# Optimization experiments

Measured on AMD Instinct MI355X. Metric: run time of the kernel, lower is better.

## Reference

```python
import jax, jax.numpy as jnp
import numpy as np

B, S, E = 2, 2048, 1024
H, HKV = 16, 4
D = E // H          # head_dim = 64
REP = H // HKV      # kv repeat factor = 4


def setup_inputs() -> dict:
    key = jax.random.key(0)
    ks = jax.random.split(key, 9)
    std = 0.02
    x = jax.random.normal(ks[0], (B, S, E), dtype=jnp.float32)
    # causal mask: True means masked (upper triangle, strictly above diagonal)
    mask = jnp.triu(jnp.ones((S, S), dtype=bool), k=1)
    wq_w = jax.random.normal(ks[1], (E, E), dtype=jnp.float32) * std
    wq_b = jax.random.normal(ks[2], (E,), dtype=jnp.float32) * std
    wk_w = jax.random.normal(ks[3], (HKV * D, E), dtype=jnp.float32) * std
    wk_b = jax.random.normal(ks[4], (HKV * D,), dtype=jnp.float32) * std
    wv_w = jax.random.normal(ks[5], (HKV * D, E), dtype=jnp.float32) * std
    wv_b = jax.random.normal(ks[6], (HKV * D,), dtype=jnp.float32) * std
    wo_w = jax.random.normal(ks[7], (E, E), dtype=jnp.float32) * std
    wo_b = jax.random.normal(ks[8], (E,), dtype=jnp.float32) * std
    return {"x": x, "mask": mask, "wq_w": wq_w, "wq_b": wq_b,
            "wk_w": wk_w, "wk_b": wk_b, "wv_w": wv_w, "wv_b": wv_b,
            "wo_w": wo_w, "wo_b": wo_b}


def reference(x, mask, wq_w, wq_b, wk_w, wk_b, wv_w, wv_b, wo_w, wo_b):
    b, s, e = x.shape
    # projections (torch Linear: x @ W.T + b)
    q = x @ wq_w.T + wq_b                       # [B,S,E]
    k = x @ wk_w.T + wk_b                       # [B,S,HKV*D]
    v = x @ wv_w.T + wv_b
    # q grouped by kv head: [B, HKV, REP, S, D]; k/v: [B, HKV, S, D]
    q = q.reshape(b, s, HKV, REP, D).transpose(0, 2, 3, 1, 4)
    k = k.reshape(b, s, HKV, D).transpose(0, 2, 1, 3)
    v = v.reshape(b, s, HKV, D).transpose(0, 2, 1, 3)
    scale = D ** (-0.5)
    # scores [B, HKV, REP, Sq, Skv] -- same math as physical repeat_kv
    scores = jnp.einsum('bgrsd,bgtd->bgrst', q, k) * scale
    scores = jnp.where(mask, -jnp.inf, scores)
    w = jax.nn.softmax(scores, axis=-1)
    ctx = jnp.einsum('bgrst,bgtd->bgrsd', w, v)  # [B,HKV,REP,S,D]
    ctx = ctx.transpose(0, 3, 1, 2, 4).reshape(b, s, e)
    return ctx @ wo_w.T + wo_b
```

## Files before the change

kernel.cpp:

```cpp
#include <hip/hip_runtime.h>


typedef __attribute__((ext_vector_type(8))) short bh8;
typedef __attribute__((ext_vector_type(4))) short sh4;
typedef __attribute__((ext_vector_type(4))) float fv4;
typedef __attribute__((ext_vector_type(2))) unsigned int uv2;

#define MFMA16 __builtin_amdgcn_mfma_f32_16x16x32_bf16

static __device__ __forceinline__ float fast_exp2(float x) {
  return __builtin_amdgcn_exp2f(x);
}
static __device__ __forceinline__ unsigned short f2bf(float f) {
  unsigned int u; __builtin_memcpy(&u, &f, 4);
  u += 0x7fffu + ((u >> 16) & 1u);
  return (unsigned short)(u >> 16);
}
static __device__ __forceinline__ unsigned int pack2(float a, float b) {
  unsigned int r;
  asm("v_cvt_pk_bf16_f32 %0, %1, %2" : "=v"(r) : "v"(a), "v"(b));
  return r;
}
static __device__ __forceinline__ void gload16(const short* g, short* l) {
  __builtin_amdgcn_global_load_lds(
      (const __attribute__((address_space(1))) void*)g,
      (__attribute__((address_space(3))) void*)l, 16, 0, 0);
}

static __device__ __forceinline__ bh8 pshuf(const float* p, int quad, int l16) {
  unsigned int u01 = pack2(p[0], p[1]);
  unsigned int u23 = pack2(p[2], p[3]);
  unsigned int u45 = pack2(p[4], p[5]);
  unsigned int u67 = pack2(p[6], p[7]);
  const int g0 = (((quad << 1)    ) & 3) * 16 + l16;
  const int g1 = (((quad << 1) + 1) & 3) * 16 + l16;
  unsigned int w0l = __shfl((int)u01, g0), w0h = __shfl((int)u45, g0);
  unsigned int w1l = __shfl((int)u23, g0), w1h = __shfl((int)u67, g0);
  unsigned int w2l = __shfl((int)u01, g1), w2h = __shfl((int)u45, g1);
  unsigned int w3l = __shfl((int)u23, g1), w3h = __shfl((int)u67, g1);
  const bool up = (quad & 2) != 0;
  union { unsigned int w[4]; bh8 v; } pu;
  pu.w[0] = up ? w0h : w0l;
  pu.w[1] = up ? w1h : w1l;
  pu.w[2] = up ? w2h : w2l;
  pu.w[3] = up ? w3h : w3l;
  return pu.v;
}

__global__ __launch_bounds__(256) void cvt_all(
    const float* __restrict__ x,  const float* __restrict__ wq,
    const float* __restrict__ wk, const float* __restrict__ wv,
    const float* __restrict__ wo,
    short* __restrict__ xb, short* __restrict__ wqkvb, short* __restrict__ wob)
{
  const int i = blockIdx.x * 256 + threadIdx.x;
  const float* src; short* dst; int j;
  if (i < 1048576)      { j = i;           src = x;  dst = xb; }
  else if (i < 1310720) { j = i - 1048576; src = wq; dst = wqkvb; }
  else if (i < 1376256) { j = i - 1310720; src = wk; dst = wqkvb + (size_t)1024 * 1024; }
  else if (i < 1441792) { j = i - 1376256; src = wv; dst = wqkvb + (size_t)1280 * 1024; }
  else                  { j = i - 1441792; src = wo; dst = wob; }
  const float4 v = ((const float4*)src)[j];
  sh4 o = { (short)f2bf(v.x), (short)f2bf(v.y),
            (short)f2bf(v.z), (short)f2bf(v.w) };
  ((sh4*)dst)[j] = o;
}

__global__ __launch_bounds__(256) void gemm_dbuf(
    const short* __restrict__ A, const short* __restrict__ W,
    const float* __restrict__ biasQ, const float* __restrict__ biasK,
    const float* __restrict__ biasV,
    short* __restrict__ Cq, short* __restrict__ Ck, short* __restrict__ Cvt,
    float* __restrict__ Cf,
    int M, int K, int S, int mode, float scaleQ)
{
  __shared__ short As[2][128 * 64];
  __shared__ short Bs[2][64 * 64];
  const int tid  = threadIdx.x;
  const int wave = tid >> 6, lane = tid & 63;
  const int quad = lane >> 4, l16 = lane & 15;
  const int row0 = blockIdx.x * 128, col0 = blockIdx.y * 64;
  const int wr = (wave >> 1) * 64, wc = (wave & 1) * 32;

  fv4 acc[4][2] = {};

  const int srow = lane >> 3;
  const int scg  = (lane & 7) ^ srow;
  const short* ag = A + (size_t)(row0 + wave * 32 + srow) * K + scg * 8;
  const short* bg = W + (size_t)(col0 + wave * 16 + srow) * K + scg * 8;

  auto stage = [&](int b, int k0) {
    #pragma unroll
    for (int e = 0; e < 4; e++)
      gload16(ag + (size_t)(e * 8) * K + k0, &As[b][(wave * 32 + e * 8) * 64]);
    #pragma unroll
    for (int e = 0; e < 2; e++)
      gload16(bg + (size_t)(e * 8) * K + k0, &Bs[b][(wave * 16 + e * 8) * 64]);
  };

  stage(0, 0);
  __syncthreads();
  const int nIter = K / 64;
  for (int it = 0; it < nIter; it++) {
    const int cur = it & 1;
    if (it + 1 < nIter) stage(cur ^ 1, (it + 1) * 64);

    #pragma unroll
    for (int kk = 0; kk < 2; kk++) {
      const int g = kk * 4 + quad;
      bh8 af[4], bf[2];
      #pragma unroll
      for (int i = 0; i < 4; i++) {
        const int r = wr + i * 16 + l16;
        af[i] = *(const bh8*)&As[cur][r * 64 + ((g ^ (r & 7)) * 8)];
      }
      #pragma unroll
      for (int j = 0; j < 2; j++) {
        const int r = wc + j * 16 + l16;
        bf[j] = *(const bh8*)&Bs[cur][r * 64 + ((g ^ (r & 7)) * 8)];
      }
      #pragma unroll
      for (int i = 0; i < 4; i++)
        #pragma unroll
        for (int j = 0; j < 2; j++)
          acc[i][j] = MFMA16(af[i], bf[j], acc[i][j], 0, 0, 0);
    }
    __syncthreads();
  }

  if (mode == 2) {
    float bv[2];
    #pragma unroll
    for (int j = 0; j < 2; j++) bv[j] = biasQ[col0 + wc + j * 16 + l16];
    #pragma unroll
    for (int i = 0; i < 4; i++) {
      const int row = row0 + wr + i * 16 + quad * 4;
      #pragma unroll
      for (int j = 0; j < 2; j++) {
        const int col = col0 + wc + j * 16 + l16;
        #pragma unroll
        for (int r = 0; r < 4; r++)
          Cf[(size_t)(row + r) * 1024 + col] = acc[i][j][r] + bv[j];
      }
    }
  } else if (col0 < 1024) {
    float bv[2];
    #pragma unroll
    for (int j = 0; j < 2; j++) bv[j] = biasQ[col0 + wc + j * 16 + l16];
    #pragma unroll
    for (int i = 0; i < 4; i++) {
      const int row = row0 + wr + i * 16 + quad * 4;
      #pragma unroll
      for (int j = 0; j < 2; j++) {
        const int col = col0 + wc + j * 16 + l16;
        #pragma unroll
        for (int r = 0; r < 4; r++)
          Cq[(size_t)(row + r) * 1024 + col] =
              (short)f2bf((acc[i][j][r] + bv[j]) * scaleQ);
      }
    }
  } else if (col0 < 1280) {
    float bv[2];
    #pragma unroll
    for (int j = 0; j < 2; j++) bv[j] = biasK[col0 + wc + j * 16 + l16 - 1024];
    #pragma unroll
    for (int i = 0; i < 4; i++) {
      const int row = row0 + wr + i * 16 + quad * 4;
      #pragma unroll
      for (int j = 0; j < 2; j++) {
        const int col = col0 + wc + j * 16 + l16 - 1024;
        #pragma unroll
        for (int r = 0; r < 4; r++)
          Ck[(size_t)(row + r) * 256 + col] = (short)f2bf(acc[i][j][r] + bv[j]);
      }
    }
  } else {
    float bv[2];
    #pragma unroll
    for (int j = 0; j < 2; j++) bv[j] = biasV[col0 + wc + j * 16 + l16 - 1280];
    const int b  = row0 / S;
    const int sb = row0 - b * S;
    #pragma unroll
    for (int i = 0; i < 4; i++) {
      const int s = sb + wr + i * 16 + quad * 4;
      #pragma unroll
      for (int j = 0; j < 2; j++) {
        const int np = col0 + wc + j * 16 + l16 - 1280;
        sh4 v = { (short)f2bf(acc[i][j][0] + bv[j]),
                  (short)f2bf(acc[i][j][1] + bv[j]),
                  (short)f2bf(acc[i][j][2] + bv[j]),
                  (short)f2bf(acc[i][j][3] + bv[j]) };
        *(sh4*)(Cvt + ((size_t)(b * 256 + np)) * S + s) = v;
      }
    }
  }
}

__global__ __launch_bounds__(256) void gqa_attn(
    const short* __restrict__ Q,
    const short* __restrict__ Kg,
    const short* __restrict__ Vt,
    short* __restrict__ ctx)
{
  const int S = 2048, E = 1024, KVE = 256;
  __shared__ short Ks[2][2][4096];
  __shared__ short Vs[2][2][4096];
  __shared__ short P2[4][2][1024];

  const int wave = threadIdx.x >> 6;
  const int lane = threadIdx.x & 63;
  const int quad = lane >> 4, l16 = lane & 15;
  const int bh = blockIdx.y;
  const int b = bh >> 4, h = bh & 15, kv = h >> 2;

  const short* Kb = Kg + (size_t)b * S * KVE + kv * 64;
  const short* Vb = Vt + ((size_t)(b * 4 + kv)) * 64 * S;
  short* PhA = &P2[wave][0][0];
  short* PhB = &P2[wave][1][0];

  const int srow = lane >> 3;
  const int scg  = (lane & 7) ^ srow;

  const int kc0 = (quad ^ (l16 & 7)) * 8;
  const int kc1 = ((quad ^ 4) ^ (l16 & 7)) * 8;
  const int l7  = l16 & 7;
  const int pwr = l16 * 64;
  const int prA = pwr + ((quad ^ l7) * 8);
  const int prB = pwr + (((4 + quad) ^ l7) * 8);

  auto stage64 = [&](int buf, int half, int t0) {
    #pragma unroll
    for (int e = 0; e < 2; e++) {
      const int g = wave * 2 + e;
      const int row = g * 8 + srow;
      gload16(Kb + (size_t)(t0 + row) * KVE + scg * 8, &Ks[buf][half][g * 512]);
      gload16(Vb + (size_t)row * S + t0 + scg * 8,     &Vs[buf][half][g * 512]);
    }
  };

  for (int ph = 0; ph < 2; ph++) {
    const int j = ph ? (31 - (int)blockIdx.x) : (int)blockIdx.x;
    const int qblk0 = j * 64;
    const int q0 = qblk0 + wave * 16;

    const short* qrow = Q + (size_t)(b * S + q0 + l16) * E + h * 64 + quad * 8;
    bh8 qf0 = *(const bh8*)(qrow);
    bh8 qf1 = *(const bh8*)(qrow + 32);

    fv4 acc0{}, acc1{}, acc2{}, acc3{};
    float rs = 0.f;

    auto qk_sub = [&](const short* ks, fv4* st) {
      __builtin_amdgcn_s_setprio(1);
      #pragma unroll
      for (int i = 0; i < 4; i++) {
        const int tb = (i * 16 + l16) * 64;
        bh8 k0 = *(const bh8*)&ks[tb + kc0];
        bh8 k1 = *(const bh8*)&ks[tb + kc1];
        st[i] = MFMA16(k0, qf0, st[i], 0, 0, 0);
        st[i] = MFMA16(k1, qf1, st[i], 0, 0, 0);
      }
      __builtin_amdgcn_s_setprio(0);
    };
    auto exppack = [&](fv4* st, short* Ph) {
      #pragma unroll
      for (int i = 0; i < 4; i++) {
        float p0 = fast_exp2(st[i][0]);
        float p1 = fast_exp2(st[i][1]);
        float p2 = fast_exp2(st[i][2]);
        float p3 = fast_exp2(st[i][3]);
        rs += (p0 + p1) + (p2 + p3);
        uv2 u = { pack2(p0, p1), pack2(p2, p3) };
        const int pg = ((i * 2 + (quad >> 1)) ^ l7) * 8 + (quad & 1) * 4;
        *(uv2*)&Ph[pwr + pg] = u;
      }
    };
    auto pv_sub = [&](const short* vs, const short* Ph) {
      bh8 pfA = *(const bh8*)&Ph[prA];
      bh8 pfB = *(const bh8*)&Ph[prB];
      __builtin_amdgcn_s_setprio(1);
      #pragma unroll
      for (int dt = 0; dt < 4; dt++) {
        const int db = (dt * 16 + l16) * 64;
        bh8 v0 = *(const bh8*)&vs[db + kc0];
        bh8 v1 = *(const bh8*)&vs[db + kc1];
        fv4* a = dt == 0 ? &acc0 : dt == 1 ? &acc1 : dt == 2 ? &acc2 : &acc3;
        *a = MFMA16(v0, pfA, *a, 0, 0, 0);
        *a = MFMA16(v1, pfB, *a, 0, 0, 0);
      }
      __builtin_amdgcn_s_setprio(0);
    };

    const int n64  = qblk0 >> 6;
    const int n128 = n64 >> 1, rem = n64 & 1;
    if (n64 > 0) {
      stage64(0, 0, 0);
      if (n128 > 0) stage64(0, 1, 64);
      for (int it = 0; it < n128; it++) {
        const int cur = it & 1;
        if (it + 1 < n128) {
          stage64(cur ^ 1, 0, (it + 1) * 128);
          stage64(cur ^ 1, 1, (it + 1) * 128 + 64);
          asm volatile("s_waitcnt vmcnt(8)" ::: "memory");
        } else if (rem) {
          stage64(cur ^ 1, 0, n128 * 128);
          asm volatile("s_waitcnt vmcnt(4)" ::: "memory");
        } else {
          asm volatile("s_waitcnt vmcnt(0)" ::: "memory");
        }
        __builtin_amdgcn_sched_barrier(0);
        __builtin_amdgcn_s_barrier();

        fv4 stA[4] = {}, stB[4] = {};
        qk_sub(&Ks[cur][0][0], stA);
        exppack(stA, PhA);
        qk_sub(&Ks[cur][1][0], stB);
        pv_sub(&Vs[cur][0][0], PhA);
        exppack(stB, PhB);
        pv_sub(&Vs[cur][1][0], PhB);

        asm volatile("s_waitcnt lgkmcnt(0)" ::: "memory");
        __builtin_amdgcn_sched_barrier(0);
        __builtin_amdgcn_s_barrier();
      }
      if (rem) {
        const int cur2 = n128 & 1;
        asm volatile("s_waitcnt vmcnt(0)" ::: "memory");
        __builtin_amdgcn_sched_barrier(0);
        __builtin_amdgcn_s_barrier();
        fv4 stA[4] = {};
        qk_sub(&Ks[cur2][0][0], stA);
        exppack(stA, PhA);
        pv_sub(&Vs[cur2][0][0], PhA);
        asm volatile("s_waitcnt lgkmcnt(0)" ::: "memory");
        __builtin_amdgcn_sched_barrier(0);
        __builtin_amdgcn_s_barrier();
      }
    }

    const int nk = q0 + 16;
    for (int t0 = qblk0; t0 < nk; t0 += 32) {
      fv4 st0{}, st1{};
      {
        const short* kr = Kb + (size_t)(t0 + l16) * KVE + quad * 8;
        bh8 k0 = *(const bh8*)(kr);
        bh8 k1 = *(const bh8*)(kr + 32);
        st0 = MFMA16(k0, qf0, st0, 0, 0, 0);
        st0 = MFMA16(k1, qf1, st0, 0, 0, 0);
      }
      const bool do2 = (t0 + 16) < nk;
      if (do2) {
        const short* kr = Kb + (size_t)(t0 + 16 + l16) * KVE + quad * 8;
        bh8 k0 = *(const bh8*)(kr);
        bh8 k1 = *(const bh8*)(kr + 32);
        st1 = MFMA16(k0, qf0, st1, 0, 0, 0);
        st1 = MFMA16(k1, qf1, st1, 0, 0, 0);
      }
      const int qg = q0 + l16;
      float p[8];
      #pragma unroll
      for (int r = 0; r < 4; r++) {
        const int t = t0 + quad * 4 + r;
        p[r]     = (t <= qg)               ? fast_exp2(st0[r]) : 0.f;
        p[4 + r] = (do2 && (t + 16) <= qg) ? fast_exp2(st1[r]) : 0.f;
      }
      #pragma unroll
      for (int i = 0; i < 8; i++) rs += p[i];

      bh8 pf = pshuf(p, quad, l16);
      const short* vr = Vb + (size_t)l16 * S + t0 + quad * 8;
      acc0 = MFMA16(*(const bh8*)(vr),          pf, acc0, 0, 0, 0);
      acc1 = MFMA16(*(const bh8*)(vr + 16 * S), pf, acc1, 0, 0, 0);
      acc2 = MFMA16(*(const bh8*)(vr + 32 * S), pf, acc2, 0, 0, 0);
      acc3 = MFMA16(*(const bh8*)(vr + 48 * S), pf, acc3, 0, 0, 0);
    }

    float lsum = rs;
    lsum += __shfl_xor(lsum, 16);
    lsum += __shfl_xor(lsum, 32);
    const float inv = 1.f / lsum;

    short* orow = ctx + (size_t)(b * S + q0 + l16) * E + h * 64 + quad * 4;
    sh4 o0 = { (short)f2bf(acc0[0] * inv), (short)f2bf(acc0[1] * inv),
               (short)f2bf(acc0[2] * inv), (short)f2bf(acc0[3] * inv) };
    sh4 o1 = { (short)f2bf(acc1[0] * inv), (short)f2bf(acc1[1] * inv),
               (short)f2bf(acc1[2] * inv), (short)f2bf(acc1[3] * inv) };
    sh4 o2 = { (short)f2bf(acc2[0] * inv), (short)f2bf(acc2[1] * inv),
               (short)f2bf(acc2[2] * inv), (short)f2bf(acc2[3] * inv) };
    sh4 o3 = { (short)f2bf(acc3[0] * inv), (short)f2bf(acc3[1] * inv),
               (short)f2bf(acc3[2] * inv), (short)f2bf(acc3[3] * inv) };
    *(sh4*)(orow)      = o0;
    *(sh4*)(orow + 16) = o1;
    *(sh4*)(orow + 32) = o2;
    *(sh4*)(orow + 48) = o3;
  }
}

extern "C" void kernel_launch(void* const* d_in, const int* in_sizes, int n_in,
                              void* d_out, int out_size, void* d_ws, size_t ws_size,
                              hipStream_t stream)
{
  const float* x    = (const float*)d_in[0];
  const float* wq_w = (const float*)d_in[2];
  const float* wq_b = (const float*)d_in[3];
  const float* wk_w = (const float*)d_in[4];
  const float* wk_b = (const float*)d_in[5];
  const float* wv_w = (const float*)d_in[6];
  const float* wv_b = (const float*)d_in[7];
  const float* wo_w = (const float*)d_in[8];
  const float* wo_b = (const float*)d_in[9];
  float* out = (float*)d_out;

  const int S = 2048, E = 1024, M = 2 * S;
  const float sl2e = 0.125f * 1.44269504f;

  char* ob = (char*)d_out;
  short* Qb   = (short*)(ob);
  short* Kbuf = (short*)(ob + (size_t)( 8 << 20));
  short* Vtb  = (short*)(ob + (size_t)(10 << 20));

  char* ws = (char*)d_ws;
  short* xb    = (short*)(ws);
  short* wqkvb = (short*)(ws + (size_t)( 8 << 20));
  short* wob   = (short*)(ws + (size_t)(11 << 20));
  short* Cx    = xb;

  dim3 blk(256);
  cvt_all<<<dim3(6656), blk, 0, stream>>>(x, wq_w, wk_w, wv_w, wo_w,
                                          xb, wqkvb, wob);
  gemm_dbuf<<<dim3(M / 128, 1536 / 64), blk, 0, stream>>>(
      xb, wqkvb, wq_b, wk_b, wv_b, Qb, Kbuf, Vtb, nullptr, M, E, S, 0, sl2e);
  gqa_attn<<<dim3(16, 2 * 16), blk, 0, stream>>>(Qb, Kbuf, Vtb, Cx);
  gemm_dbuf<<<dim3(M / 128, 1024 / 64), blk, 0, stream>>>(
      Cx, wob, wo_b, nullptr, nullptr, nullptr, nullptr, nullptr, out,
      M, E, S, 2, 1.f);
}
```

Before: 168.1 us.

## Share staged K/V tiles between both paired query blocks in one pass

Each block handles a query block j and its mirror 31-j. Before, it ran two separate passes, each staging K/V tiles from global into LDS. Now it makes a single pass over the longer block's K/V range, and the shorter block computes on the same staged tiles while they are still inside its causal range. This halves the global-to-LDS traffic for the shared prefix and removes one set of pipeline warmups, at the cost of more live registers (two Q fragments and two accumulator sets) and a more complex P-buffer interleave.

After: 170.2 us. Within noise of the previous version (+1.3%).

```diff
diff --git a/kernel.cpp b/kernel.cpp
--- a/kernel.cpp
+++ b/kernel.cpp
@@ -215,8 +215,8 @@
 
   const short* Kb = Kg + (size_t)b * S * KVE + kv * 64;
   const short* Vb = Vt + ((size_t)(b * 4 + kv)) * 64 * S;
-  short* PhA = &P2[wave][0][0];
-  short* PhB = &P2[wave][1][0];
+  short* PhX = &P2[wave][0][0];
+  short* PhY = &P2[wave][1][0];
 
   const int srow = lane >> 3;
   const int scg  = (lane & 7) ^ srow;
@@ -238,105 +238,121 @@
     }
   };
 
-  for (int ph = 0; ph < 2; ph++) {
-    const int j = ph ? (31 - (int)blockIdx.x) : (int)blockIdx.x;
-    const int qblk0 = j * 64;
-    const int q0 = qblk0 + wave * 16;
-
-    const short* qrow = Q + (size_t)(b * S + q0 + l16) * E + h * 64 + quad * 8;
-    bh8 qf0 = *(const bh8*)(qrow);
-    bh8 qf1 = *(const bh8*)(qrow + 32);
-
-    fv4 acc0{}, acc1{}, acc2{}, acc3{};
-    float rs = 0.f;
-
-    auto qk_sub = [&](const short* ks, fv4* st) {
-      __builtin_amdgcn_s_setprio(1);
-      #pragma unroll
-      for (int i = 0; i < 4; i++) {
-        const int tb = (i * 16 + l16) * 64;
-        bh8 k0 = *(const bh8*)&ks[tb + kc0];
-        bh8 k1 = *(const bh8*)&ks[tb + kc1];
-        st[i] = MFMA16(k0, qf0, st[i], 0, 0, 0);
-        st[i] = MFMA16(k1, qf1, st[i], 0, 0, 0);
-      }
-      __builtin_amdgcn_s_setprio(0);
-    };
-    auto exppack = [&](fv4* st, short* Ph) {
-      #pragma unroll
-      for (int i = 0; i < 4; i++) {
-        float p0 = fast_exp2(st[i][0]);
-        float p1 = fast_exp2(st[i][1]);
-        float p2 = fast_exp2(st[i][2]);
-        float p3 = fast_exp2(st[i][3]);
-        rs += (p0 + p1) + (p2 + p3);
-        uv2 u = { pack2(p0, p1), pack2(p2, p3) };
-        const int pg = ((i * 2 + (quad >> 1)) ^ l7) * 8 + (quad & 1) * 4;
-        *(uv2*)&Ph[pwr + pg] = u;
-      }
-    };
-    auto pv_sub = [&](const short* vs, const short* Ph) {
-      bh8 pfA = *(const bh8*)&Ph[prA];
-      bh8 pfB = *(const bh8*)&Ph[prB];
-      __builtin_amdgcn_s_setprio(1);
-      #pragma unroll
-      for (int dt = 0; dt < 4; dt++) {
-        const int db = (dt * 16 + l16) * 64;
-        bh8 v0 = *(const bh8*)&vs[db + kc0];
-        bh8 v1 = *(const bh8*)&vs[db + kc1];
-        fv4* a = dt == 0 ? &acc0 : dt == 1 ? &acc1 : dt == 2 ? &acc2 : &acc3;
-        *a = MFMA16(v0, pfA, *a, 0, 0, 0);
-        *a = MFMA16(v1, pfB, *a, 0, 0, 0);
-      }
-      __builtin_amdgcn_s_setprio(0);
-    };
-
-    const int n64  = qblk0 >> 6;
-    const int n128 = n64 >> 1, rem = n64 & 1;
-    if (n64 > 0) {
-      stage64(0, 0, 0);
-      if (n128 > 0) stage64(0, 1, 64);
-      for (int it = 0; it < n128; it++) {
-        const int cur = it & 1;
-        if (it + 1 < n128) {
-          stage64(cur ^ 1, 0, (it + 1) * 128);
-          stage64(cur ^ 1, 1, (it + 1) * 128 + 64);
-          asm volatile("s_waitcnt vmcnt(8)" ::: "memory");
-        } else if (rem) {
-          stage64(cur ^ 1, 0, n128 * 128);
-          asm volatile("s_waitcnt vmcnt(4)" ::: "memory");
-        } else {
-          asm volatile("s_waitcnt vmcnt(0)" ::: "memory");
-        }
-        __builtin_amdgcn_sched_barrier(0);
-        __builtin_amdgcn_s_barrier();
-
-        fv4 stA[4] = {}, stB[4] = {};
-        qk_sub(&Ks[cur][0][0], stA);
-        exppack(stA, PhA);
-        qk_sub(&Ks[cur][1][0], stB);
-        pv_sub(&Vs[cur][0][0], PhA);
-        exppack(stB, PhB);
-        pv_sub(&Vs[cur][1][0], PhB);
-
-        asm volatile("s_waitcnt lgkmcnt(0)" ::: "memory");
-        __builtin_amdgcn_sched_barrier(0);
-        __builtin_amdgcn_s_barrier();
-      }
-      if (rem) {
-        const int cur2 = n128 & 1;
-        asm volatile("s_waitcnt vmcnt(0)" ::: "memory");
-        __builtin_amdgcn_sched_barrier(0);
-        __builtin_amdgcn_s_barrier();
-        fv4 stA[4] = {};
-        qk_sub(&Ks[cur2][0][0], stA);
-        exppack(stA, PhA);
-        pv_sub(&Vs[cur2][0][0], PhA);
-        asm volatile("s_waitcnt lgkmcnt(0)" ::: "memory");
-        __builtin_amdgcn_sched_barrier(0);
-        __builtin_amdgcn_s_barrier();
-      }
-    }
+  const int j0 = (int)blockIdx.x;
+  const int j1 = 31 - j0;
+  const int lim0 = j0 * 64;
+  const int q00 = lim0 + wave * 16;
+  const int q01 = j1 * 64 + wave * 16;
+
+  const short* qr0 = Q + (size_t)(b * S + q00 + l16) * E + h * 64 + quad * 8;
+  const short* qr1 = Q + (size_t)(b * S + q01 + l16) * E + h * 64 + quad * 8;
+  bh8 qa0 = *(const bh8*)(qr0), qa1 = *(const bh8*)(qr0 + 32);
+  bh8 qb0 = *(const bh8*)(qr1), qb1 = *(const bh8*)(qr1 + 32);
+
+  fv4 accP0[4] = {}; fv4 accP1[4] = {};
+  float rs0 = 0.f, rs1 = 0.f;
+
+  auto qk_sub = [&](const short* ks, bh8 qf0, bh8 qf1, fv4* st) {
+    __builtin_amdgcn_s_setprio(1);
+    #pragma unroll
+    for (int i = 0; i < 4; i++) {
+      const int tb = (i * 16 + l16) * 64;
+      bh8 k0 = *(const bh8*)&ks[tb + kc0];
+      bh8 k1 = *(const bh8*)&ks[tb + kc1];
+      st[i] = MFMA16(k0, qf0, st[i], 0, 0, 0);
+      st[i] = MFMA16(k1, qf1, st[i], 0, 0, 0);
+    }
+    __builtin_amdgcn_s_setprio(0);
+  };
+  auto exppack = [&](fv4* st, short* Ph, float& rs) {
+    #pragma unroll
+    for (int i = 0; i < 4; i++) {
+      float p0 = fast_exp2(st[i][0]);
+      float p1 = fast_exp2(st[i][1]);
+      float p2 = fast_exp2(st[i][2]);
+      float p3 = fast_exp2(st[i][3]);
+      rs += (p0 + p1) + (p2 + p3);
+      uv2 u = { pack2(p0, p1), pack2(p2, p3) };
+      const int pg = ((i * 2 + (quad >> 1)) ^ l7) * 8 + (quad & 1) * 4;
+      *(uv2*)&Ph[pwr + pg] = u;
+    }
+  };
+  auto pv_sub = [&](const short* vs, const short* Ph, fv4* acc) {
+    bh8 pfA = *(const bh8*)&Ph[prA];
+    bh8 pfB = *(const bh8*)&Ph[prB];
+    __builtin_amdgcn_s_setprio(1);
+    #pragma unroll
+    for (int dt = 0; dt < 4; dt++) {
+      const int db = (dt * 16 + l16) * 64;
+      bh8 v0 = *(const bh8*)&vs[db + kc0];
+      bh8 v1 = *(const bh8*)&vs[db + kc1];
+      fv4* a = dt == 0 ? &acc[0] : dt == 1 ? &acc[1] : dt == 2 ? &acc[2] : &acc[3];
+      *a = MFMA16(v0, pfA, *a, 0, 0, 0);
+      *a = MFMA16(v1, pfB, *a, 0, 0, 0);
+    }
+    __builtin_amdgcn_s_setprio(0);
+  };
+
+  const int n128 = j1 >> 1, rem = j1 & 1;
+  stage64(0, 0, 0);
+  stage64(0, 1, 64);
+  for (int it = 0; it < n128; it++) {
+    const int cur = it & 1;
+    if (it + 1 < n128) {
+      stage64(cur ^ 1, 0, (it + 1) * 128);
+      stage64(cur ^ 1, 1, (it + 1) * 128 + 64);
+      asm volatile("s_waitcnt vmcnt(8)" ::: "memory");
+    } else if (rem) {
+      stage64(cur ^ 1, 0, n128 * 128);
+      asm volatile("s_waitcnt vmcnt(4)" ::: "memory");
+    } else {
+      asm volatile("s_waitcnt vmcnt(0)" ::: "memory");
+    }
+    __builtin_amdgcn_sched_barrier(0);
+    __builtin_amdgcn_s_barrier();
+
+    const int tA = it * 128;
+    const bool dA0 = tA < lim0;
+    const bool dB0 = (tA + 64) < lim0;
+    fv4 stA1[4] = {}, stA0[4] = {}, stB1[4] = {}, stB0[4] = {};
+
+    qk_sub(&Ks[cur][0][0], qb0, qb1, stA1);
+    exppack(stA1, PhX, rs1);
+    if (dA0) { qk_sub(&Ks[cur][0][0], qa0, qa1, stA0);
+               exppack(stA0, PhY, rs0); }
+    qk_sub(&Ks[cur][1][0], qb0, qb1, stB1);
+    if (dB0)   qk_sub(&Ks[cur][1][0], qa0, qa1, stB0);
+    if (!dA0)  exppack(stB1, PhY, rs1);
+    pv_sub(&Vs[cur][0][0], PhX, accP1);
+    if (dA0)   exppack(stB1, PhX, rs1);
+    if (dA0)   pv_sub(&Vs[cur][0][0], PhY, accP0);
+    if (dB0)   exppack(stB0, PhY, rs0);
+    pv_sub(&Vs[cur][1][0], dA0 ? PhX : PhY, accP1);
+    if (dB0)   pv_sub(&Vs[cur][1][0], PhY, accP0);
+
+    asm volatile("s_waitcnt lgkmcnt(0)" ::: "memory");
+    __builtin_amdgcn_sched_barrier(0);
+    __builtin_amdgcn_s_barrier();
+  }
+  if (rem) {
+    const int cur2 = n128 & 1;
+    asm volatile("s_waitcnt vmcnt(0)" ::: "memory");
+    __builtin_amdgcn_sched_barrier(0);
+    __builtin_amdgcn_s_barrier();
+    fv4 stA1[4] = {};
+    qk_sub(&Ks[cur2][0][0], qb0, qb1, stA1);
+    exppack(stA1, PhX, rs1);
+    pv_sub(&Vs[cur2][0][0], PhX, accP1);
+  }
+
+  #pragma unroll
+  for (int phx = 0; phx < 2; phx++) {
+    const int qblk0 = phx ? j1 * 64 : lim0;
+    const int q0    = phx ? q01 : q00;
+    const bh8 qf0   = phx ? qb0 : qa0;
+    const bh8 qf1   = phx ? qb1 : qa1;
+    fv4* acc  = phx ? accP1 : accP0;
+    float rs  = phx ? rs1 : rs0;
 
     const int nk = q0 + 16;
     for (int t0 = qblk0; t0 < nk; t0 += 32) {
@@ -369,10 +385,10 @@
 
       bh8 pf = pshuf(p, quad, l16);
       const short* vr = Vb + (size_t)l16 * S + t0 + quad * 8;
-      acc0 = MFMA16(*(const bh8*)(vr),          pf, acc0, 0, 0, 0);
-      acc1 = MFMA16(*(const bh8*)(vr + 16 * S), pf, acc1, 0, 0, 0);
-      acc2 = MFMA16(*(const bh8*)(vr + 32 * S), pf, acc2, 0, 0, 0);
-      acc3 = MFMA16(*(const bh8*)(vr + 48 * S), pf, acc3, 0, 0, 0);
+      acc[0] = MFMA16(*(const bh8*)(vr),          pf, acc[0], 0, 0, 0);
+      acc[1] = MFMA16(*(const bh8*)(vr + 16 * S), pf, acc[1], 0, 0, 0);
+      acc[2] = MFMA16(*(const bh8*)(vr + 32 * S), pf, acc[2], 0, 0, 0);
+      acc[3] = MFMA16(*(const bh8*)(vr + 48 * S), pf, acc[3], 0, 0, 0);
     }
 
     float lsum = rs;
@@ -381,18 +397,12 @@
     const float inv = 1.f / lsum;
 
     short* orow = ctx + (size_t)(b * S + q0 + l16) * E + h * 64 + quad * 4;
-    sh4 o0 = { (short)f2bf(acc0[0] * inv), (short)f2bf(acc0[1] * inv),
-               (short)f2bf(acc0[2] * inv), (short)f2bf(acc0[3] * inv) };
-    sh4 o1 = { (short)f2bf(acc1[0] * inv), (short)f2bf(acc1[1] * inv),
-               (short)f2bf(acc1[2] * inv), (short)f2bf(acc1[3] * inv) };
-    sh4 o2 = { (short)f2bf(acc2[0] * inv), (short)f2bf(acc2[1] * inv),
-               (short)f2bf(acc2[2] * inv), (short)f2bf(acc2[3] * inv) };
-    sh4 o3 = { (short)f2bf(acc3[0] * inv), (short)f2bf(acc3[1] * inv),
-               (short)f2bf(acc3[2] * inv), (short)f2bf(acc3[3] * inv) };
-    *(sh4*)(orow)      = o0;
-    *(sh4*)(orow + 16) = o1;
-    *(sh4*)(orow + 32) = o2;
-    *(sh4*)(orow + 48) = o3;
+    #pragma unroll
+    for (int i = 0; i < 4; i++) {
+      sh4 o = { (short)f2bf(acc[i][0] * inv), (short)f2bf(acc[i][1] * inv),
+                (short)f2bf(acc[i][2] * inv), (short)f2bf(acc[i][3] * inv) };
+      *(sh4*)(orow + i * 16) = o;
+    }
   }
 }
 
```
